# Optimization experiments

Measured on AMD Instinct MI355X. Metric: run time of the kernel, lower is better.

The kernel has to match this reference:

```python
import jax, jax.numpy as jnp
import numpy as np

HEAD_SIZE = 64
N_EMBD = 128
B, T = 16, 2048


def setup_inputs() -> dict:
    key = jax.random.key(0)
    ks = jax.random.split(key, 7)
    s = 1.0 / np.sqrt(N_EMBD)
    return {
        "x": jax.random.normal(ks[0], (B, T, N_EMBD), dtype=jnp.float32),
        "Wk": jax.random.normal(ks[1], (N_EMBD, HEAD_SIZE), dtype=jnp.float32) * s,
        "bk": jax.random.normal(ks[2], (HEAD_SIZE,), dtype=jnp.float32) * s,
        "Wq": jax.random.normal(ks[3], (N_EMBD, HEAD_SIZE), dtype=jnp.float32) * s,
        "bq": jax.random.normal(ks[4], (HEAD_SIZE,), dtype=jnp.float32) * s,
        "Wv": jax.random.normal(ks[5], (N_EMBD, HEAD_SIZE), dtype=jnp.float32) * s,
        "bv": jax.random.normal(ks[6], (HEAD_SIZE,), dtype=jnp.float32) * s,
    }


def reference(x, Wk, bk, Wq, bq, Wv, bv):
    # x: [B, T, C]; single-head causal attention (dropout in eval mode = identity)
    Tdim = x.shape[1]
    k = x @ Wk + bk  # [B, T, H]
    q = x @ Wq + bq  # [B, T, H]
    v = x @ Wv + bv  # [B, T, H]
    scale = jnp.asarray(k.shape[-1], x.dtype) ** -0.5
    wei = jnp.einsum("bth,bsh->bts", q, k) * scale  # [B, T, T]
    causal = jnp.tril(jnp.ones((Tdim, Tdim), dtype=bool))
    wei = jnp.where(causal, wei, -jnp.inf)
    wei = jax.nn.softmax(wei, axis=-1)
    out = jnp.einsum("bts,bsh->bth", wei, v)  # [B, T, H]
    return out
```

## Files before the change

kernel.cpp:

```cpp
#include <hip/hip_runtime.h>
#include <hip/hip_bf16.h>
#include <math.h>

#define HS 64
#define NE 128
#define TSEQ 2048

typedef short s8v __attribute__((ext_vector_type(8)));
typedef float f4v __attribute__((ext_vector_type(4)));

__device__ __forceinline__ unsigned short f2bf(float f) {
    unsigned int u = __float_as_uint(f);
    u += 0x7FFFu + ((u >> 16) & 1u);
    return (unsigned short)(u >> 16);
}

__device__ __forceinline__ float bf2f(unsigned short h) {
    return __uint_as_float(((unsigned int)h) << 16);
}

__device__ __forceinline__ unsigned int pkbf(float a, float b) {
    union { __hip_bfloat162 h; unsigned int u; } cv;
    cv.h = __float22bfloat162_rn(make_float2(a, b));
    return cv.u;
}

__device__ __forceinline__ s8v mk_s8v(unsigned int a, unsigned int b,
                                      unsigned int c, unsigned int d) {
    union { unsigned int u[4]; s8v v; } cv;
    cv.u[0] = a; cv.u[1] = b; cv.u[2] = c; cv.u[3] = d;
    return cv.v;
}

__device__ __forceinline__ float fexp2(float x) {
    float r;
    asm("v_exp_f32 %0, %1" : "=v"(r) : "v"(x));
    return r;
}

__device__ __forceinline__ void glds16(const unsigned short* g, unsigned short* l) {
    __builtin_amdgcn_global_load_lds(
        (const __attribute__((address_space(1))) unsigned int*)g,
        (__attribute__((address_space(3))) unsigned int*)l,
        16, 0, 0);
}

__global__ __launch_bounds__(256) void wconv(
    const float* __restrict__ Wq, const float* __restrict__ Wk,
    const float* __restrict__ Wv, unsigned short* __restrict__ wt)
{
    const int o0 = (blockIdx.x * 256 + threadIdx.x) * 2;
    const int mat = o0 >> 13;
    const int n = (o0 >> 7) & 63;
    const int k = o0 & 127;
    const float* W = (mat == 0) ? Wq : (mat == 1) ? Wk : Wv;
    const float s = (mat == 0) ? 0.18033688f : 1.0f;
    unsigned int lo = f2bf(W[k * HS + n] * s);
    unsigned int hi = f2bf(W[(k + 1) * HS + n] * s);
    *(unsigned int*)(wt + o0) = lo | (hi << 16);
}

__global__ __launch_bounds__(256) void qkv(
    const float* __restrict__ x, const unsigned short* __restrict__ wt,
    const float* __restrict__ bq, const float* __restrict__ bk,
    const float* __restrict__ bv,
    unsigned short* __restrict__ qo, unsigned short* __restrict__ ko,
    unsigned short* __restrict__ vt)
{
    __shared__ __align__(16) unsigned short Ws[192 * 136];

    const int tid = threadIdx.x;
    const int w = tid >> 6;
    const int lane = tid & 63;
    const int quad = lane >> 4;
    const int li = lane & 15;
    const size_t blk0 = (size_t)blockIdx.x * 64;
    const size_t row0w = blk0 + (size_t)w * 16;

#pragma unroll
    for (int p = 0; p < 12; ++p) {
        const int idx = p * 256 + tid;
        const int n = idx >> 4;
        const int c = idx & 15;
        s8v d = *(const s8v*)(wt + idx * 8);
        *(s8v*)&Ws[n * 136 + c * 8] = d;
    }

    s8v a[4];
    const float* xr = x + (row0w + li) * NE + quad * 8;
#pragma unroll
    for (int ks = 0; ks < 4; ++ks) {
        float4 f0 = *(const float4*)(xr + ks * 32);
        float4 f1 = *(const float4*)(xr + ks * 32 + 4);
        a[ks] = mk_s8v(pkbf(f0.x, f0.y), pkbf(f0.z, f0.w),
                       pkbf(f1.x, f1.y), pkbf(f1.z, f1.w));
    }

    __syncthreads();

    f4v acc[12];
#pragma unroll
    for (int nt = 0; nt < 12; ++nt) acc[nt] = (f4v){0.f, 0.f, 0.f, 0.f};

#pragma unroll
    for (int nt = 0; nt < 12; ++nt) {
        const unsigned short* wr = &Ws[(nt * 16 + li) * 136 + quad * 8];
#pragma unroll
        for (int ks = 0; ks < 4; ++ks) {
            s8v bfr = *(const s8v*)(wr + ks * 32);
            acc[nt] = __builtin_amdgcn_mfma_f32_16x16x32_bf16(a[ks], bfr, acc[nt], 0, 0, 0);
        }
    }

    const size_t bidx = row0w >> 11;
    const size_t trow0 = row0w & 2047;
#pragma unroll
    for (int nt = 0; nt < 4; ++nt) {
        const float bias = bv[nt * 16 + li];
        unsigned int lo = pkbf(acc[nt + 8][0] + bias, acc[nt + 8][1] + bias);
        unsigned int hi = pkbf(acc[nt + 8][2] + bias, acc[nt + 8][3] + bias);
        *(uint2*)(vt + (bidx * HS + nt * 16 + li) * TSEQ + trow0 + quad * 4) =
            make_uint2(lo, hi);
    }

    __syncthreads();

    float* Qt = (float*)Ws;
    float* Kt = Qt + 64 * 68;
    const float sq = 0.18033688f;
    const int lrow0 = w * 16 + quad * 4;
#pragma unroll
    for (int nt = 0; nt < 4; ++nt) {
        const int col = nt * 16 + li;
        const float bq_ = bq[col] * sq;
        const float bk_ = bk[col];
#pragma unroll
        for (int r = 0; r < 4; ++r) {
            Qt[(lrow0 + r) * 68 + col] = acc[nt][r] + bq_;
            Kt[(lrow0 + r) * 68 + col] = acc[nt + 4][r] + bk_;
        }
    }

    __syncthreads();

    const int row = tid >> 2;
    const int seg = tid & 3;
    {
        const float* src = &Qt[row * 68 + seg * 16];
        float4 f0 = *(const float4*)src;
        float4 f1 = *(const float4*)(src + 4);
        float4 f2 = *(const float4*)(src + 8);
        float4 f3 = *(const float4*)(src + 12);
        s8v d0 = mk_s8v(pkbf(f0.x, f0.y), pkbf(f0.z, f0.w), pkbf(f1.x, f1.y), pkbf(f1.z, f1.w));
        s8v d1 = mk_s8v(pkbf(f2.x, f2.y), pkbf(f2.z, f2.w), pkbf(f3.x, f3.y), pkbf(f3.z, f3.w));
        unsigned short* dst = qo + (blk0 + row) * HS + seg * 16;
        *(s8v*)dst = d0;
        *(s8v*)(dst + 8) = d1;
    }
    {
        const float* src = &Kt[row * 68 + seg * 16];
        float4 f0 = *(const float4*)src;
        float4 f1 = *(const float4*)(src + 4);
        float4 f2 = *(const float4*)(src + 8);
        float4 f3 = *(const float4*)(src + 12);
        s8v d0 = mk_s8v(pkbf(f0.x, f0.y), pkbf(f0.z, f0.w), pkbf(f1.x, f1.y), pkbf(f1.z, f1.w));
        s8v d1 = mk_s8v(pkbf(f2.x, f2.y), pkbf(f2.z, f2.w), pkbf(f3.x, f3.y), pkbf(f3.z, f3.w));
        unsigned short* dst = ko + (blk0 + row) * HS + seg * 16;
        *(s8v*)dst = d0;
        *(s8v*)(dst + 8) = d1;
    }
}

__device__ __forceinline__ void attn_tile_group(
    const unsigned short* Kc, const unsigned short* Vc,
    char* pbse, int lane, int quad, int li, int swz0, int swz1,
    int tl, int dg, int qrow, s8v qf0, s8v qf1, f4v* c_o, float& lsum)
{
    float pr[4][4];
    float rs = 0.f;
#pragma unroll
    for (int kt = 0; kt < 4; ++kt) {
        const unsigned short* krow = Kc + (kt * 16 + li) * 64;
        s8v k0 = *(const s8v*)(krow + swz0);
        s8v k1 = *(const s8v*)(krow + swz1);
        f4v cst = (f4v){0.f, 0.f, 0.f, 0.f};
        __builtin_amdgcn_s_setprio(1);
        cst = __builtin_amdgcn_mfma_f32_16x16x32_bf16(k0, qf0, cst, 0, 0, 0);
        cst = __builtin_amdgcn_mfma_f32_16x16x32_bf16(k1, qf1, cst, 0, 0, 0);
        __builtin_amdgcn_s_setprio(0);
        if (tl == dg) {
            const int key0 = (tl << 6) + kt * 16 + quad * 4;
#pragma unroll
            for (int rr = 0; rr < 4; ++rr)
                if (key0 + rr > qrow) cst[rr] = -INFINITY;
        }
#pragma unroll
        for (int rr = 0; rr < 4; ++rr) {
            pr[kt][rr] = fexp2(cst[rr]);
            rs += pr[kt][rr];
        }
    }
    lsum += rs;

#pragma unroll
    for (int kt = 0; kt < 4; ++kt) {
        *(uint2*)(pbse + (kt * 2 + (quad >> 1)) * 256 + li * 16 + (quad & 1) * 8) =
            make_uint2(pkbf(pr[kt][0], pr[kt][1]), pkbf(pr[kt][2], pr[kt][3]));
    }
    s8v pf0 = *(const s8v*)(pbse + lane * 16);
    s8v pf1 = *(const s8v*)(pbse + 1024 + lane * 16);

#pragma unroll
    for (int f = 0; f < 4; ++f) {
        const unsigned short* vrow = Vc + (f * 16 + li) * 64;
        s8v v0 = *(const s8v*)(vrow + swz0);
        s8v v1 = *(const s8v*)(vrow + swz1);
        __builtin_amdgcn_s_setprio(1);
        c_o[f] = __builtin_amdgcn_mfma_f32_16x16x32_bf16(v0, pf0, c_o[f], 0, 0, 0);
        c_o[f] = __builtin_amdgcn_mfma_f32_16x16x32_bf16(v1, pf1, c_o[f], 0, 0, 0);
        __builtin_amdgcn_s_setprio(0);
    }
}

__global__ __launch_bounds__(256) void attn_main(
    const unsigned short* __restrict__ qbf,
    const unsigned short* __restrict__ kb,
    const unsigned short* __restrict__ vtb,
    float* __restrict__ out, unsigned short* __restrict__ pbf,
    float* __restrict__ lsbuf)
{
    __shared__ unsigned short Ks[2][64 * 64];
    __shared__ unsigned short Vs[2][64 * 64];
    __shared__ __align__(16) unsigned short Ps[4][1024];

    const int tid = threadIdx.x;
    const int w = tid >> 6;
    const int lane = tid & 63;
    const int quad = lane >> 4;
    const int li = lane & 15;

    const int id = blockIdx.x;
    const int xcd = id & 7;
    const int j = id >> 3;
    const int b = xcd * 2 + (j >= 72);
    const int jj = (j >= 72) ? j - 72 : j;
    const int u = 71 - jj;

    int m = 0;
    while ((m + 1) * (m + 2) <= u) ++m;
    const int rem = u - m * (m + 1);
    const int qb = 2 * m + (rem > m ? 1 : 0);
    const int c = (rem > m) ? rem - (m + 1) : rem;
    const int nc = m + 1;
    const int tb = c * 4;
    const int ntile = 2 * qb + 2;
    const int te = (tb + 4 < ntile) ? tb + 4 : ntile;

    const size_t base = (size_t)b * TSEQ;
    const int t0 = qb << 7;
    const int qrow0 = t0 + w * 16 + li;
    const int qrow1 = qrow0 + 64;
    const int d0 = 2 * qb;
    const int d1 = 2 * qb + 1;

    const unsigned short* qrp0 = qbf + (base + qrow0) * HS + quad * 8;
    s8v qA0 = *(const s8v*)qrp0;
    s8v qA1 = *(const s8v*)(qrp0 + 32);
    const unsigned short* qrp1 = qrp0 + 64 * HS;
    s8v qB0 = *(const s8v*)qrp1;
    s8v qB1 = *(const s8v*)(qrp1 + 32);

    const int rA = w * 8 + (lane >> 3);
    const int csw = (lane & 7) ^ (rA & 7);
    const unsigned short* kgA = kb + (base + rA) * HS + csw * 8;
    const unsigned short* kgB = kgA + 32 * HS;
    const unsigned short* vgA = vtb + ((size_t)b * HS + rA) * TSEQ + csw * 8;
    const unsigned short* vgB = vgA + 32 * TSEQ;
    const int ldsA = w * 512 + lane * 8;
    const int ldsB = 2048 + w * 512 + lane * 8;

    glds16(kgA + (size_t)tb * 4096, &Ks[0][ldsA]);
    glds16(kgB + (size_t)tb * 4096, &Ks[0][ldsB]);
    glds16(vgA + (size_t)tb * 64,   &Vs[0][ldsA]);
    glds16(vgB + (size_t)tb * 64,   &Vs[0][ldsB]);

    f4v c_oA[4], c_oB[4];
#pragma unroll
    for (int f = 0; f < 4; ++f) {
        c_oA[f] = (f4v){0.f, 0.f, 0.f, 0.f};
        c_oB[f] = (f4v){0.f, 0.f, 0.f, 0.f};
    }
    float lsA = 0.f, lsB = 0.f;

    char* pbse = (char*)&Ps[w][0];
    const int swz0 = (quad ^ (li & 7)) * 8;
    const int swz1 = ((4 + quad) ^ (li & 7)) * 8;

    __syncthreads();

    for (int tl = tb; tl < te; ++tl) {
        const int bi = (tl - tb) & 1;
        if (tl + 1 < te) {
            const int nb = bi ^ 1;
            glds16(kgA + (size_t)(tl + 1) * 4096, &Ks[nb][ldsA]);
            glds16(kgB + (size_t)(tl + 1) * 4096, &Ks[nb][ldsB]);
            glds16(vgA + (size_t)(tl + 1) * 64,   &Vs[nb][ldsA]);
            glds16(vgB + (size_t)(tl + 1) * 64,   &Vs[nb][ldsB]);
        }
        const unsigned short* Kc = &Ks[bi][0];
        const unsigned short* Vc = &Vs[bi][0];

        if (tl <= d0)
            attn_tile_group(Kc, Vc, pbse, lane, quad, li, swz0, swz1,
                            tl, d0, qrow0, qA0, qA1, c_oA, lsA);
        attn_tile_group(Kc, Vc, pbse, lane, quad, li, swz0, swz1,
                        tl, d1, qrow1, qB0, qB1, c_oB, lsB);

        __syncthreads();
    }

    lsA += __shfl_xor(lsA, 16);
    lsA += __shfl_xor(lsA, 32);
    lsB += __shfl_xor(lsB, 16);
    lsB += __shfl_xor(lsB, 32);

    if (nc == 1) {
        const float invA = 1.0f / lsA;
        float* orowA = out + (base + qrow0) * HS + quad * 4;
#pragma unroll
        for (int f = 0; f < 4; ++f) {
            f4v res = c_oA[f];
            res[0] *= invA; res[1] *= invA; res[2] *= invA; res[3] *= invA;
            *(f4v*)(orowA + f * 16) = res;
        }
        const float invB = 1.0f / lsB;
        float* orowB = out + (base + qrow1) * HS + quad * 4;
#pragma unroll
        for (int f = 0; f < 4; ++f) {
            f4v res = c_oB[f];
            res[0] *= invB; res[1] *= invB; res[2] *= invB; res[3] *= invB;
            *(f4v*)(orowB + f * 16) = res;
        }
    } else {
        const int pidx = b * 70 + (u - 2);
        unsigned short* pc = pbf + (size_t)pidx * 8192 + (w * 16 + li) * 64;
#pragma unroll
        for (int f = 0; f < 4; ++f) {
            *(uint2*)(pc + f * 16 + quad * 4) =
                make_uint2(pkbf(c_oA[f][0], c_oA[f][1]), pkbf(c_oA[f][2], c_oA[f][3]));
        }
        unsigned short* pc1 = pc + 64 * 64;
#pragma unroll
        for (int f = 0; f < 4; ++f) {
            *(uint2*)(pc1 + f * 16 + quad * 4) =
                make_uint2(pkbf(c_oB[f][0], c_oB[f][1]), pkbf(c_oB[f][2], c_oB[f][3]));
        }
        if (quad == 0) {
            lsbuf[(size_t)pidx * 128 + w * 16 + li] = lsA;
            lsbuf[(size_t)pidx * 128 + 64 + w * 16 + li] = lsB;
        }
    }
}

__global__ __launch_bounds__(256) void attn_reduce(
    const unsigned short* __restrict__ pbf, const float* __restrict__ lsbuf,
    float* __restrict__ out)
{
    const int g = blockIdx.x;
    const int b = g / 28;
    const int rem = g - b * 28;
    const int r = 2 + (rem >> 1);
    const int half = rem & 1;
    const int m = r >> 1;
    const int nc = m + 1;
    const int pidx0 = b * 70 + m * (m + 1) + (r & 1) * (m + 1) - 2;

    const int tid = threadIdx.x;
    const int row = half * 64 + (tid >> 2);
    const int seg = tid & 3;

    float acc[16];
#pragma unroll
    for (int k = 0; k < 16; ++k) acc[k] = 0.f;
    float ls = 0.f;

    for (int cc = 0; cc < nc; ++cc) {
        const unsigned short* ps = pbf + (size_t)(pidx0 + cc) * 8192 + row * 64 + seg * 16;
        s8v v0 = *(const s8v*)ps;
        s8v v1 = *(const s8v*)(ps + 8);
#pragma unroll
        for (int e = 0; e < 8; ++e) {
            acc[e] += bf2f((unsigned short)v0[e]);
            acc[8 + e] += bf2f((unsigned short)v1[e]);
        }
        ls += lsbuf[(size_t)(pidx0 + cc) * 128 + row];
    }
    const float inv = 1.0f / ls;
    float* orow = out + ((size_t)b * TSEQ + (r << 7) + row) * HS + seg * 16;
#pragma unroll
    for (int jj = 0; jj < 4; ++jj) {
        *(float4*)(orow + jj * 4) = make_float4(acc[jj * 4] * inv,
                                                acc[jj * 4 + 1] * inv,
                                                acc[jj * 4 + 2] * inv,
                                                acc[jj * 4 + 3] * inv);
    }
}

extern "C" void kernel_launch(void* const* d_in, const int* in_sizes, int n_in,
                              void* d_out, int out_size, void* d_ws, size_t ws_size,
                              hipStream_t stream) {
    const float* x  = (const float*)d_in[0];
    const float* Wk = (const float*)d_in[1];
    const float* bk = (const float*)d_in[2];
    const float* Wq = (const float*)d_in[3];
    const float* bq = (const float*)d_in[4];
    const float* Wv = (const float*)d_in[5];
    const float* bv = (const float*)d_in[6];
    float* outp = (float*)d_out;

    const size_t elems = (size_t)16 * TSEQ * HS;
    unsigned short* qbuf = (unsigned short*)d_ws;
    unsigned short* kbuf = qbuf + elems;
    unsigned short* vbuf = kbuf + elems;
    unsigned short* wtb  = vbuf + elems;
    unsigned short* pbf  = wtb + 32768;
    float* lsbuf = (float*)(pbf + (size_t)1120 * 8192);

    wconv<<<48, 256, 0, stream>>>(Wq, Wk, Wv, wtb);
    qkv<<<512, 256, 0, stream>>>(x, wtb, bq, bk, bv, qbuf, kbuf, vbuf);
    attn_main<<<1152, 256, 0, stream>>>(qbuf, kbuf, vbuf, outp, pbf, lsbuf);
    attn_reduce<<<448, 256, 0, stream>>>(pbf, lsbuf, outp);
}
```

Measured before the change: 114.3 us.

## Fold weight conversion into qkv and single-buffer K/V tiles in attention

Removes the separate weight-conversion kernel: each qkv block reads the fp32 weights directly, scales and converts them to bf16 while filling shared memory. In attn_main the K/V shared buffers go from double to single, the next tile is loaded after compute behind an extra barrier, and launch bounds ask for 4 blocks per CU. This cuts one launch and shared memory per block to raise occupancy. The cost is that the load/compute overlap inside a block is lost and every qkv block repeats the weight conversion with strided fp32 reads.

```diff
diff --git a/kernel.cpp b/kernel.cpp
--- a/kernel.cpp
+++ b/kernel.cpp
@@ -8,12 +8,6 @@
 
 typedef short s8v __attribute__((ext_vector_type(8)));
 typedef float f4v __attribute__((ext_vector_type(4)));
-
-__device__ __forceinline__ unsigned short f2bf(float f) {
-    unsigned int u = __float_as_uint(f);
-    u += 0x7FFFu + ((u >> 16) & 1u);
-    return (unsigned short)(u >> 16);
-}
 
 __device__ __forceinline__ float bf2f(unsigned short h) {
     return __uint_as_float(((unsigned int)h) << 16);
@@ -45,23 +39,10 @@
         16, 0, 0);
 }
 
-__global__ __launch_bounds__(256) void wconv(
+__global__ __launch_bounds__(256) void qkv(
+    const float* __restrict__ x,
     const float* __restrict__ Wq, const float* __restrict__ Wk,
-    const float* __restrict__ Wv, unsigned short* __restrict__ wt)
-{
-    const int o0 = (blockIdx.x * 256 + threadIdx.x) * 2;
-    const int mat = o0 >> 13;
-    const int n = (o0 >> 7) & 63;
-    const int k = o0 & 127;
-    const float* W = (mat == 0) ? Wq : (mat == 1) ? Wk : Wv;
-    const float s = (mat == 0) ? 0.18033688f : 1.0f;
-    unsigned int lo = f2bf(W[k * HS + n] * s);
-    unsigned int hi = f2bf(W[(k + 1) * HS + n] * s);
-    *(unsigned int*)(wt + o0) = lo | (hi << 16);
-}
-
-__global__ __launch_bounds__(256) void qkv(
-    const float* __restrict__ x, const unsigned short* __restrict__ wt,
+    const float* __restrict__ Wv,
     const float* __restrict__ bq, const float* __restrict__ bk,
     const float* __restrict__ bv,
     unsigned short* __restrict__ qo, unsigned short* __restrict__ ko,
@@ -80,10 +61,16 @@
 #pragma unroll
     for (int p = 0; p < 12; ++p) {
         const int idx = p * 256 + tid;
-        const int n = idx >> 4;
+        const int ng = idx >> 4;
         const int c = idx & 15;
-        s8v d = *(const s8v*)(wt + idx * 8);
-        *(s8v*)&Ws[n * 136 + c * 8] = d;
+        const float* Wsrc = (ng < 64) ? Wq : (ng < 128) ? Wk : Wv;
+        const float s = (ng < 64) ? 0.18033688f : 1.0f;
+        const float* wp = Wsrc + c * 8 * 64 + (ng & 63);
+        unsigned int u0 = pkbf(wp[0] * s,   wp[64] * s);
+        unsigned int u1 = pkbf(wp[128] * s, wp[192] * s);
+        unsigned int u2 = pkbf(wp[256] * s, wp[320] * s);
+        unsigned int u3 = pkbf(wp[384] * s, wp[448] * s);
+        *(s8v*)&Ws[ng * 136 + c * 8] = mk_s8v(u0, u1, u2, u3);
     }
 
     s8v a[4];
@@ -222,15 +209,15 @@
     }
 }
 
-__global__ __launch_bounds__(256) void attn_main(
+__global__ __launch_bounds__(256, 4) void attn_main(
     const unsigned short* __restrict__ qbf,
     const unsigned short* __restrict__ kb,
     const unsigned short* __restrict__ vtb,
     float* __restrict__ out, unsigned short* __restrict__ pbf,
     float* __restrict__ lsbuf)
 {
-    __shared__ unsigned short Ks[2][64 * 64];
-    __shared__ unsigned short Vs[2][64 * 64];
+    __shared__ unsigned short Ks[64 * 64];
+    __shared__ unsigned short Vs[64 * 64];
     __shared__ __align__(16) unsigned short Ps[4][1024];
 
     const int tid = threadIdx.x;
@@ -279,10 +266,10 @@
     const int ldsA = w * 512 + lane * 8;
     const int ldsB = 2048 + w * 512 + lane * 8;
 
-    glds16(kgA + (size_t)tb * 4096, &Ks[0][ldsA]);
-    glds16(kgB + (size_t)tb * 4096, &Ks[0][ldsB]);
-    glds16(vgA + (size_t)tb * 64,   &Vs[0][ldsA]);
-    glds16(vgB + (size_t)tb * 64,   &Vs[0][ldsB]);
+    glds16(kgA + (size_t)tb * 4096, &Ks[ldsA]);
+    glds16(kgB + (size_t)tb * 4096, &Ks[ldsB]);
+    glds16(vgA + (size_t)tb * 64,   &Vs[ldsA]);
+    glds16(vgB + (size_t)tb * 64,   &Vs[ldsB]);
 
     f4v c_oA[4], c_oB[4];
 #pragma unroll
@@ -299,24 +286,21 @@
     __syncthreads();
 
     for (int tl = tb; tl < te; ++tl) {
-        const int bi = (tl - tb) & 1;
+        if (tl <= d0)
+            attn_tile_group(Ks, Vs, pbse, lane, quad, li, swz0, swz1,
+                            tl, d0, qrow0, qA0, qA1, c_oA, lsA);
+        attn_tile_group(Ks, Vs, pbse, lane, quad, li, swz0, swz1,
+                        tl, d1, qrow1, qB0, qB1, c_oB, lsB);
+
+        __syncthreads();
+
         if (tl + 1 < te) {
-            const int nb = bi ^ 1;
-            glds16(kgA + (size_t)(tl + 1) * 4096, &Ks[nb][ldsA]);
-            glds16(kgB + (size_t)(tl + 1) * 4096, &Ks[nb][ldsB]);
-            glds16(vgA + (size_t)(tl + 1) * 64,   &Vs[nb][ldsA]);
-            glds16(vgB + (size_t)(tl + 1) * 64,   &Vs[nb][ldsB]);
-        }
-        const unsigned short* Kc = &Ks[bi][0];
-        const unsigned short* Vc = &Vs[bi][0];
-
-        if (tl <= d0)
-            attn_tile_group(Kc, Vc, pbse, lane, quad, li, swz0, swz1,
-                            tl, d0, qrow0, qA0, qA1, c_oA, lsA);
-        attn_tile_group(Kc, Vc, pbse, lane, quad, li, swz0, swz1,
-                        tl, d1, qrow1, qB0, qB1, c_oB, lsB);
-
-        __syncthreads();
+            glds16(kgA + (size_t)(tl + 1) * 4096, &Ks[ldsA]);
+            glds16(kgB + (size_t)(tl + 1) * 4096, &Ks[ldsB]);
+            glds16(vgA + (size_t)(tl + 1) * 64,   &Vs[ldsA]);
+            glds16(vgB + (size_t)(tl + 1) * 64,   &Vs[ldsB]);
+            __syncthreads();
+        }
     }
 
     lsA += __shfl_xor(lsA, 16);
@@ -422,12 +406,10 @@
     unsigned short* qbuf = (unsigned short*)d_ws;
     unsigned short* kbuf = qbuf + elems;
     unsigned short* vbuf = kbuf + elems;
-    unsigned short* wtb  = vbuf + elems;
-    unsigned short* pbf  = wtb + 32768;
+    unsigned short* pbf  = vbuf + elems;
     float* lsbuf = (float*)(pbf + (size_t)1120 * 8192);
 
-    wconv<<<48, 256, 0, stream>>>(Wq, Wk, Wv, wtb);
-    qkv<<<512, 256, 0, stream>>>(x, wtb, bq, bk, bv, qbuf, kbuf, vbuf);
+    qkv<<<512, 256, 0, stream>>>(x, Wq, Wk, Wv, bq, bk, bv, qbuf, kbuf, vbuf);
     attn_main<<<1152, 256, 0, stream>>>(qbuf, kbuf, vbuf, outp, pbf, lsbuf);
     attn_reduce<<<448, 256, 0, stream>>>(pbf, lsbuf, outp);
 }
```

New measurement: 128.0 us. +12.0%, slower.

## Single-buffer V tile with mid-iteration barrier and raise occupancy hint

Applied to the files above, without the earlier changes.

The V tile goes from double-buffered to single-buffered in shared memory. It is now loaded at the start of each iteration, and a new barrier sits between the first group's QK^T step and its PV step. The attention tile routine is split into separate QK and PV helpers, and launch bounds ask for 4 blocks per SM. The aim is lower LDS use and higher occupancy, but the V load is no longer prefetched a tile ahead. The extra barrier's wait may also stall on the in-flight K prefetch, exposing memory latency.

```diff
diff --git a/kernel.cpp b/kernel.cpp
--- a/kernel.cpp
+++ b/kernel.cpp
@@ -171,10 +171,10 @@
     }
 }
 
-__device__ __forceinline__ void attn_tile_group(
-    const unsigned short* Kc, const unsigned short* Vc,
-    char* pbse, int lane, int quad, int li, int swz0, int swz1,
-    int tl, int dg, int qrow, s8v qf0, s8v qf1, f4v* c_o, float& lsum)
+__device__ __forceinline__ void attn_qk(
+    const unsigned short* Kc, char* pbse, int lane, int quad, int li,
+    int swz0, int swz1, int tl, int dg, int qrow,
+    s8v qf0, s8v qf1, float& lsum, s8v& pf0, s8v& pf1)
 {
     float pr[4][4];
     float rs = 0.f;
@@ -207,9 +207,14 @@
         *(uint2*)(pbse + (kt * 2 + (quad >> 1)) * 256 + li * 16 + (quad & 1) * 8) =
             make_uint2(pkbf(pr[kt][0], pr[kt][1]), pkbf(pr[kt][2], pr[kt][3]));
     }
-    s8v pf0 = *(const s8v*)(pbse + lane * 16);
-    s8v pf1 = *(const s8v*)(pbse + 1024 + lane * 16);
-
+    pf0 = *(const s8v*)(pbse + lane * 16);
+    pf1 = *(const s8v*)(pbse + 1024 + lane * 16);
+}
+
+__device__ __forceinline__ void attn_pv(
+    const unsigned short* Vc, int li, int swz0, int swz1,
+    s8v pf0, s8v pf1, f4v* c_o)
+{
 #pragma unroll
     for (int f = 0; f < 4; ++f) {
         const unsigned short* vrow = Vc + (f * 16 + li) * 64;
@@ -222,7 +227,7 @@
     }
 }
 
-__global__ __launch_bounds__(256) void attn_main(
+__global__ __launch_bounds__(256, 4) void attn_main(
     const unsigned short* __restrict__ qbf,
     const unsigned short* __restrict__ kb,
     const unsigned short* __restrict__ vtb,
@@ -230,7 +235,7 @@
     float* __restrict__ lsbuf)
 {
     __shared__ unsigned short Ks[2][64 * 64];
-    __shared__ unsigned short Vs[2][64 * 64];
+    __shared__ unsigned short Vs[64 * 64];
     __shared__ __align__(16) unsigned short Ps[4][1024];
 
     const int tid = threadIdx.x;
@@ -281,8 +286,6 @@
 
     glds16(kgA + (size_t)tb * 4096, &Ks[0][ldsA]);
     glds16(kgB + (size_t)tb * 4096, &Ks[0][ldsB]);
-    glds16(vgA + (size_t)tb * 64,   &Vs[0][ldsA]);
-    glds16(vgB + (size_t)tb * 64,   &Vs[0][ldsB]);
 
     f4v c_oA[4], c_oB[4];
 #pragma unroll
@@ -300,21 +303,29 @@
 
     for (int tl = tb; tl < te; ++tl) {
         const int bi = (tl - tb) & 1;
+        glds16(vgA + (size_t)tl * 64, &Vs[ldsA]);
+        glds16(vgB + (size_t)tl * 64, &Vs[ldsB]);
         if (tl + 1 < te) {
             const int nb = bi ^ 1;
             glds16(kgA + (size_t)(tl + 1) * 4096, &Ks[nb][ldsA]);
             glds16(kgB + (size_t)(tl + 1) * 4096, &Ks[nb][ldsB]);
-            glds16(vgA + (size_t)(tl + 1) * 64,   &Vs[nb][ldsA]);
-            glds16(vgB + (size_t)(tl + 1) * 64,   &Vs[nb][ldsB]);
         }
         const unsigned short* Kc = &Ks[bi][0];
-        const unsigned short* Vc = &Vs[bi][0];
-
-        if (tl <= d0)
-            attn_tile_group(Kc, Vc, pbse, lane, quad, li, swz0, swz1,
-                            tl, d0, qrow0, qA0, qA1, c_oA, lsA);
-        attn_tile_group(Kc, Vc, pbse, lane, quad, li, swz0, swz1,
-                        tl, d1, qrow1, qB0, qB1, c_oB, lsB);
+        const bool doA = (tl <= d0);
+
+        s8v pfA0, pfA1, pfB0, pfB1;
+        if (doA)
+            attn_qk(Kc, pbse, lane, quad, li, swz0, swz1,
+                    tl, d0, qrow0, qA0, qA1, lsA, pfA0, pfA1);
+
+        __syncthreads();
+
+        if (doA)
+            attn_pv(Vs, li, swz0, swz1, pfA0, pfA1, c_oA);
+
+        attn_qk(Kc, pbse, lane, quad, li, swz0, swz1,
+                tl, d1, qrow1, qB0, qB1, lsB, pfB0, pfB1);
+        attn_pv(Vs, li, swz0, swz1, pfB0, pfB1, c_oB);
 
         __syncthreads();
     }
```

After: 110.8 us (median of 2 runs). -3.0%, faster.
